# Performance work log

Hardware: AMD Instinct MI355X
Metric: run time of the kernel (lower is better)

Reference implementation:

```python
import jax, jax.numpy as jnp
import numpy as np

EPS = 1e-8
SMALL = 1e-3


def _skew(v):
    # v: [B,3] -> [B,3,3]
    vx, vy, vz = v[:, 0], v[:, 1], v[:, 2]
    z = jnp.zeros_like(vx)
    row0 = jnp.stack([z, -vz, vy], axis=-1)
    row1 = jnp.stack([vz, z, -vx], axis=-1)
    row2 = jnp.stack([-vy, vx, z], axis=-1)
    return jnp.stack([row0, row1, row2], axis=-2)


def rotmat_axis_angle_stable(aa):
    # aa: [B,3] axis*angle -> [B,3,3], Taylor-stable near theta=0
    theta = jnp.linalg.norm(aa, axis=1)
    theta2 = theta * theta + EPS
    A = jnp.sin(theta) / (theta + EPS)
    Bc = (1.0 - jnp.cos(theta)) / theta2
    th2 = theta * theta
    th4 = th2 * th2
    small = theta < SMALL
    A = jnp.where(small, 1.0 - th2 / 6.0 + th4 / 120.0, A)
    Bc = jnp.where(small, 0.5 - th2 / 24.0 + th4 / 720.0, Bc)
    K = _skew(aa)
    I = jnp.eye(3, dtype=aa.dtype)
    return I + A[:, None, None] * K + Bc[:, None, None] * jnp.matmul(K, K)


def _euler_to_rot(rpy):
    # rpy: [J,3] -> [J,3,3] (URDF origin rotations, constants)
    r, p, y = rpy[:, 0], rpy[:, 1], rpy[:, 2]
    cr, sr = jnp.cos(r), jnp.sin(r)
    cp, sp = jnp.cos(p), jnp.sin(p)
    cy, sy = jnp.cos(y), jnp.sin(y)
    row0 = jnp.stack([cy * cp, cy * sp * sr - sy * cr, cy * sp * cr + sy * sr], -1)
    row1 = jnp.stack([sy * cp, sy * sp * sr + cy * cr, sy * sp * cr - cy * sr], -1)
    row2 = jnp.stack([-sp, cp * sr, cp * cr], -1)
    return jnp.stack([row0, row1, row2], axis=-2)


def setup_inputs() -> dict:
    key = jax.random.key(0)
    k1, k2, k3, k4 = jax.random.split(key, 4)
    B, J = 131072, 24
    joint_angles = jax.random.normal(k1, (B, J), dtype=jnp.float32)
    # URDF origin constants: small offsets + rotations per joint
    xyz = 0.1 * jax.random.normal(k2, (J, 3), dtype=jnp.float32)
    rpy = 0.3 * jax.random.normal(k3, (J, 3), dtype=jnp.float32)
    R = _euler_to_rot(rpy)                                      # [J,3,3]
    T_origins = jnp.tile(jnp.eye(4, dtype=jnp.float32), (J, 1, 1))
    T_origins = T_origins.at[:, :3, :3].set(R).at[:, :3, 3].set(xyz)
    ax = jax.random.normal(k4, (J, 3), dtype=jnp.float32)
    axes = ax / jnp.linalg.norm(ax, axis=1, keepdims=True)      # unit axes
    return {"joint_angles": joint_angles, "T_origins": T_origins, "axes": axes}


def reference(joint_angles, T_origins, axes) -> jnp.ndarray:
    # joint_angles: [B,J]; T_origins: [J,4,4]; axes: [J,3]
    joint_angles = joint_angles.astype(jnp.float32)
    B = joint_angles.shape[0]
    eye4 = jnp.eye(4, dtype=jnp.float32)

    def step(T_parent, xs):
        T_org, axis, ang = xs                     # [4,4], [3], [B]
        aa = axis[None, :] * ang[:, None]         # [B,3]
        Rj = rotmat_axis_angle_stable(aa)         # [B,3,3]
        Tj = jnp.broadcast_to(eye4, (B, 4, 4)).at[:, :3, :3].set(Rj)
        T_child = jnp.matmul(jnp.matmul(T_parent, T_org), Tj)   # [B,4,4]
        return T_child, T_child[:, :3, 3]

    T0 = jnp.broadcast_to(eye4, (B, 4, 4))
    xs = (T_origins, axes, joint_angles.T)        # scan over J joints
    _, pos = jax.lax.scan(step, T0, xs)           # pos: [J,B,3]
    base_pos = jnp.zeros((B, 3), dtype=jnp.float32)
    pos = jnp.transpose(pos, (1, 0, 2)).reshape(B, -1)          # [B,J*3]
    return jnp.concatenate([base_pos, pos], axis=1)             # [B,(J+1)*3]
```

## Files before the change

kernel.cpp:

```cpp
#include <hip/hip_runtime.h>

#define BLK 256
#define NJ 24
#define G 8
#define NG (NJ / G)
#define NWV (BLK / 64)

typedef float vf4 __attribute__((ext_vector_type(4)));

__device__ __forceinline__ void hw_sincos(float h, float& s, float& c) {
    const float t = h * 0.15915494309189535f;
    float tf, ss, cc;
    asm("v_fract_f32 %0, %1" : "=v"(tf) : "v"(t));
    asm("v_sin_f32 %0, %1"   : "=v"(ss) : "v"(tf));
    asm("v_cos_f32 %0, %1"   : "=v"(cc) : "v"(tf));
    s = ss; c = cc;
}

__global__ __launch_bounds__(BLK, 2)
void fk_kernel(const float* __restrict__ angles,
               const float* __restrict__ Torg,
               const float* __restrict__ axes,
               float* __restrict__ out,
               int B)
{
    __shared__ float stage[BLK * 75];
    __shared__ float sP[NWV][NJ * 4];
    __shared__ float sQ[NWV][NJ * 4];
    __shared__ float sOT[NWV][NJ * 4];

    const int tid  = threadIdx.x;
    const int lane = tid & 63;
    const int wv   = tid >> 6;
    const int b    = blockIdx.x * BLK + tid;

    const float4* ap = reinterpret_cast<const float4*>(angles + (size_t)b * NJ);
    const float4 av0 = ap[0], av1 = ap[1], av2 = ap[2];
    const float4 av3 = ap[3], av4 = ap[4], av5 = ap[5];

    if (lane < NJ) {
        const float* o = Torg + lane * 16;
        const float m01=o[1], m02=o[2];
        const float m10=o[4], m12=o[6];
        const float m20=o[8], m21=o[9];
        const float tr = o[0] + o[5] + o[10];

        const float S    = 2.f * __builtin_amdgcn_sqrtf(tr + 1.f);
        const float rS   = __builtin_amdgcn_rcpf(S);
        const float qw   = 0.25f * S;
        const float qx   = (m21 - m12) * rS;
        const float qy   = (m02 - m20) * rS;
        const float qz   = (m10 - m01) * rS;

        const float axx = axes[lane*3+0], axy = axes[lane*3+1], axz = axes[lane*3+2];
        const float Qw_ = -qx*axx - qy*axy - qz*axz;
        const float Qx_ =  qw*axx + qy*axz - qz*axy;
        const float Qy_ =  qw*axy - qx*axz + qz*axx;
        const float Qz_ =  qw*axz + qx*axy - qy*axx;

        float* p = &sP[wv][lane * 4];
        p[0] = qw; p[1] = qx; p[2] = qy; p[3] = qz;
        float* q = &sQ[wv][lane * 4];
        q[0] = Qw_; q[1] = Qx_; q[2] = Qy_; q[3] = Qz_;
        float* t = &sOT[wv][lane * 4];
        t[0] = o[3]; t[1] = o[7]; t[2] = o[11]; t[3] = 0.f;
    }

    float Qw = 1.f, Qx = 0.f, Qy = 0.f, Qz = 0.f;
    float tx = 0.f, ty = 0.f, tz = 0.f;

    float* srow = &stage[tid * 75];
    srow[0] = 0.f; srow[1] = 0.f; srow[2] = 0.f;

    #pragma unroll 1
    for (int g = 0; g < NG; ++g) {
        float a[G];
        if (g == 0) {
            a[0]=av0.x; a[1]=av0.y; a[2]=av0.z; a[3]=av0.w;
            a[4]=av1.x; a[5]=av1.y; a[6]=av1.z; a[7]=av1.w;
        } else if (g == 1) {
            a[0]=av2.x; a[1]=av2.y; a[2]=av2.z; a[3]=av2.w;
            a[4]=av3.x; a[5]=av3.y; a[6]=av3.z; a[7]=av3.w;
        } else {
            a[0]=av4.x; a[1]=av4.y; a[2]=av4.z; a[3]=av4.w;
            a[4]=av5.x; a[5]=av5.y; a[6]=av5.z; a[7]=av5.w;
        }

        float U[G][4];
        float OT[G][3];
        #pragma unroll
        for (int u = 0; u < G; ++u) {
            const int j = g * G + u;
            const float4 P  = *reinterpret_cast<const float4*>(&sP[wv][j*4]);
            const float4 Qv = *reinterpret_cast<const float4*>(&sQ[wv][j*4]);
            const float4 ot = *reinterpret_cast<const float4*>(&sOT[wv][j*4]);
            OT[u][0] = ot.x; OT[u][1] = ot.y; OT[u][2] = ot.z;

            float s, c;
            hw_sincos(0.5f * a[u], s, c);

            U[u][0] = c*P.x + s*Qv.x;
            U[u][1] = c*P.y + s*Qv.y;
            U[u][2] = c*P.z + s*Qv.z;
            U[u][3] = c*P.w + s*Qv.w;
        }

        #pragma unroll
        for (int u = 0; u < G; ++u) {
            const int j = g * G + u;
            const float ox = OT[u][0], oy = OT[u][1], oz = OT[u][2];

            const float cx = Qy*oz - Qz*oy + Qw*ox;
            const float cy = Qz*ox - Qx*oz + Qw*oy;
            const float cz = Qx*oy - Qy*ox + Qw*oz;
            const float dx = Qy*cz - Qz*cy;
            const float dy = Qz*cx - Qx*cz;
            const float dz = Qx*cy - Qy*cx;
            tx = tx + ox + 2.f*dx;
            ty = ty + oy + 2.f*dy;
            tz = tz + oz + 2.f*dz;

            const float uw = U[u][0], ux = U[u][1], uy = U[u][2], uz = U[u][3];
            const float nw = Qw*uw - Qx*ux - Qy*uy - Qz*uz;
            const float nx = Qw*ux + Qx*uw + Qy*uz - Qz*uy;
            const float ny = Qw*uy - Qx*uz + Qy*uw + Qz*ux;
            const float nz = Qw*uz + Qx*uy - Qy*ux + Qz*uw;
            Qw = nw; Qx = nx; Qy = ny; Qz = nz;

            srow[3 + 3*j + 0] = tx;
            srow[3 + 3*j + 1] = ty;
            srow[3 + 3*j + 2] = tz;
        }
    }

    {
        const int rowbase = wv * 64;
        float* obase = out + ((size_t)blockIdx.x * BLK + rowbase) * 75;
        vf4* out4 = reinterpret_cast<vf4*>(obase);
        const vf4* st4 = reinterpret_cast<const vf4*>(&stage[rowbase * 75]);
        #pragma unroll
        for (int k = 0; k < 18; ++k) {
            const vf4 v = st4[lane + k * 64];
            __builtin_nontemporal_store(v, &out4[lane + k * 64]);
        }
        if (lane < 1200 - 18 * 64) {
            const vf4 v = st4[lane + 18 * 64];
            __builtin_nontemporal_store(v, &out4[lane + 18 * 64]);
        }
    }
}

extern "C" void kernel_launch(void* const* d_in, const int* in_sizes, int n_in,
                              void* d_out, int out_size, void* d_ws, size_t ws_size,
                              hipStream_t stream) {
    const float* angles = (const float*)d_in[0];
    const float* Torg   = (const float*)d_in[1];
    const float* axes   = (const float*)d_in[2];
    float* out = (float*)d_out;

    const int B = in_sizes[0] / NJ;
    const int grid = (B + BLK - 1) / BLK;

    fk_kernel<<<grid, BLK, 0, stream>>>(angles, Torg, axes, out, B);
}
```

Before: 17.83 us.

## Split each row's joint chain across 4 lanes with shuffle-based prefix scan

```diff
diff --git a/kernel.cpp b/kernel.cpp
--- a/kernel.cpp
+++ b/kernel.cpp
@@ -2,8 +2,8 @@
 
 #define BLK 256
 #define NJ 24
-#define G 8
-#define NG (NJ / G)
+#define JPL 6
+#define RPB (BLK / 4)
 #define NWV (BLK / 64)
 
 typedef float vf4 __attribute__((ext_vector_type(4)));
@@ -17,14 +17,31 @@
     s = ss; c = cc;
 }
 
-__global__ __launch_bounds__(BLK, 2)
+__device__ __forceinline__ void qtcompose(
+    float aw, float ax, float ay, float az, float atx, float aty, float atz,
+    float bw, float bx, float by, float bz, float btx, float bty, float btz,
+    float& ow, float& ox, float& oy, float& oz, float& otx, float& oty, float& otz)
+{
+    const float cx = ay*btz - az*bty + aw*btx;
+    const float cy = az*btx - ax*btz + aw*bty;
+    const float cz = ax*bty - ay*btx + aw*btz;
+    otx = atx + btx + 2.f*(ay*cz - az*cy);
+    oty = aty + bty + 2.f*(az*cx - ax*cz);
+    otz = atz + btz + 2.f*(ax*cy - ay*cx);
+    ow = aw*bw - ax*bx - ay*by - az*bz;
+    ox = aw*bx + ax*bw + ay*bz - az*by;
+    oy = aw*by - ax*bz + ay*bw + az*bx;
+    oz = aw*bz + ax*by - ay*bx + az*bw;
+}
+
+__global__ __launch_bounds__(BLK, 4)
 void fk_kernel(const float* __restrict__ angles,
                const float* __restrict__ Torg,
                const float* __restrict__ axes,
                float* __restrict__ out,
                int B)
 {
-    __shared__ float stage[BLK * 75];
+    __shared__ __align__(16) float stage[RPB * 75];
     __shared__ float sP[NWV][NJ * 4];
     __shared__ float sQ[NWV][NJ * 4];
     __shared__ float sOT[NWV][NJ * 4];
@@ -32,11 +49,12 @@
     const int tid  = threadIdx.x;
     const int lane = tid & 63;
     const int wv   = tid >> 6;
-    const int b    = blockIdx.x * BLK + tid;
+    const int q    = tid & 3;
+    const int rib  = tid >> 2;
+    const size_t row = (size_t)blockIdx.x * RPB + rib;
 
-    const float4* ap = reinterpret_cast<const float4*>(angles + (size_t)b * NJ);
-    const float4 av0 = ap[0], av1 = ap[1], av2 = ap[2];
-    const float4 av3 = ap[3], av4 = ap[4], av5 = ap[5];
+    const float2* ap2 = reinterpret_cast<const float2*>(angles + row * NJ + q * JPL);
+    const float2 a01 = ap2[0], a23 = ap2[1], a45 = ap2[2];
 
     if (lane < NJ) {
         const float* o = Torg + lane * 16;
@@ -44,108 +62,108 @@
         const float m10=o[4], m12=o[6];
         const float m20=o[8], m21=o[9];
         const float tr = o[0] + o[5] + o[10];
-
-        const float S    = 2.f * __builtin_amdgcn_sqrtf(tr + 1.f);
-        const float rS   = __builtin_amdgcn_rcpf(S);
-        const float qw   = 0.25f * S;
-        const float qx   = (m21 - m12) * rS;
-        const float qy   = (m02 - m20) * rS;
-        const float qz   = (m10 - m01) * rS;
+        const float S  = 2.f * __builtin_amdgcn_sqrtf(tr + 1.f);
+        const float rS = __builtin_amdgcn_rcpf(S);
+        const float qw = 0.25f * S;
+        const float qx = (m21 - m12) * rS;
+        const float qy = (m02 - m20) * rS;
+        const float qz = (m10 - m01) * rS;
 
         const float axx = axes[lane*3+0], axy = axes[lane*3+1], axz = axes[lane*3+2];
-        const float Qw_ = -qx*axx - qy*axy - qz*axz;
-        const float Qx_ =  qw*axx + qy*axz - qz*axy;
-        const float Qy_ =  qw*axy - qx*axz + qz*axx;
-        const float Qz_ =  qw*axz + qx*axy - qy*axx;
-
         float* p = &sP[wv][lane * 4];
         p[0] = qw; p[1] = qx; p[2] = qy; p[3] = qz;
-        float* q = &sQ[wv][lane * 4];
-        q[0] = Qw_; q[1] = Qx_; q[2] = Qy_; q[3] = Qz_;
+        float* qq = &sQ[wv][lane * 4];
+        qq[0] = -qx*axx - qy*axy - qz*axz;
+        qq[1] =  qw*axx + qy*axz - qz*axy;
+        qq[2] =  qw*axy - qx*axz + qz*axx;
+        qq[3] =  qw*axz + qx*axy - qy*axx;
         float* t = &sOT[wv][lane * 4];
         t[0] = o[3]; t[1] = o[7]; t[2] = o[11]; t[3] = 0.f;
     }
 
-    float Qw = 1.f, Qx = 0.f, Qy = 0.f, Qz = 0.f;
-    float tx = 0.f, ty = 0.f, tz = 0.f;
+    const float a[JPL] = {a01.x, a01.y, a23.x, a23.y, a45.x, a45.y};
 
-    float* srow = &stage[tid * 75];
-    srow[0] = 0.f; srow[1] = 0.f; srow[2] = 0.f;
+    float lqw[JPL], lqx[JPL], lqy[JPL], lqz[JPL];
+    float ltx[JPL], lty[JPL], ltz[JPL];
+    float Qw, Qx, Qy, Qz, Tx, Ty, Tz;
+    #pragma unroll
+    for (int u = 0; u < JPL; ++u) {
+        const int j = q * JPL + u;
+        const float4 P  = *reinterpret_cast<const float4*>(&sP[wv][j*4]);
+        const float4 Qv = *reinterpret_cast<const float4*>(&sQ[wv][j*4]);
+        const float4 ot = *reinterpret_cast<const float4*>(&sOT[wv][j*4]);
+        float s, c;
+        hw_sincos(0.5f * a[u], s, c);
+        const float uw = c*P.x + s*Qv.x;
+        const float ux = c*P.y + s*Qv.y;
+        const float uy = c*P.z + s*Qv.z;
+        const float uz = c*P.w + s*Qv.w;
+        if (u == 0) {
+            Qw = uw; Qx = ux; Qy = uy; Qz = uz;
+            Tx = ot.x; Ty = ot.y; Tz = ot.z;
+        } else {
+            float nw, nx, ny, nz, ntx, nty, ntz;
+            qtcompose(Qw,Qx,Qy,Qz,Tx,Ty,Tz, uw,ux,uy,uz,ot.x,ot.y,ot.z,
+                      nw,nx,ny,nz,ntx,nty,ntz);
+            Qw=nw; Qx=nx; Qy=ny; Qz=nz; Tx=ntx; Ty=nty; Tz=ntz;
+        }
+        lqw[u]=Qw; lqx[u]=Qx; lqy[u]=Qy; lqz[u]=Qz;
+        ltx[u]=Tx; lty[u]=Ty; ltz[u]=Tz;
+    }
 
-    #pragma unroll 1
-    for (int g = 0; g < NG; ++g) {
-        float a[G];
-        if (g == 0) {
-            a[0]=av0.x; a[1]=av0.y; a[2]=av0.z; a[3]=av0.w;
-            a[4]=av1.x; a[5]=av1.y; a[6]=av1.z; a[7]=av1.w;
-        } else if (g == 1) {
-            a[0]=av2.x; a[1]=av2.y; a[2]=av2.z; a[3]=av2.w;
-            a[4]=av3.x; a[5]=av3.y; a[6]=av3.z; a[7]=av3.w;
-        } else {
-            a[0]=av4.x; a[1]=av4.y; a[2]=av4.z; a[3]=av4.w;
-            a[4]=av5.x; a[5]=av5.y; a[6]=av5.z; a[7]=av5.w;
+    float Sw=Qw, Sx=Qx, Sy=Qy, Sz=Qz, Stx=Tx, Sty=Ty, Stz=Tz;
+    {
+        const float rw=__shfl_up(Sw,1,4), rx=__shfl_up(Sx,1,4), ry=__shfl_up(Sy,1,4), rz=__shfl_up(Sz,1,4);
+        const float rtx=__shfl_up(Stx,1,4), rty=__shfl_up(Sty,1,4), rtz=__shfl_up(Stz,1,4);
+        if (q >= 1) {
+            float ow,ox,oy,oz,otx,oty,otz;
+            qtcompose(rw,rx,ry,rz,rtx,rty,rtz, Sw,Sx,Sy,Sz,Stx,Sty,Stz, ow,ox,oy,oz,otx,oty,otz);
+            Sw=ow; Sx=ox; Sy=oy; Sz=oz; Stx=otx; Sty=oty; Stz=otz;
         }
+    }
+    {
+        const float rw=__shfl_up(Sw,2,4), rx=__shfl_up(Sx,2,4), ry=__shfl_up(Sy,2,4), rz=__shfl_up(Sz,2,4);
+        const float rtx=__shfl_up(Stx,2,4), rty=__shfl_up(Sty,2,4), rtz=__shfl_up(Stz,2,4);
+        if (q >= 2) {
+            float ow,ox,oy,oz,otx,oty,otz;
+            qtcompose(rw,rx,ry,rz,rtx,rty,rtz, Sw,Sx,Sy,Sz,Stx,Sty,Stz, ow,ox,oy,oz,otx,oty,otz);
+            Sw=ow; Sx=ox; Sy=oy; Sz=oz; Stx=otx; Sty=oty; Stz=otz;
+        }
+    }
+    float Ew=__shfl_up(Sw,1,4), Ex=__shfl_up(Sx,1,4), Ey=__shfl_up(Sy,1,4), Ez=__shfl_up(Sz,1,4);
+    float Etx=__shfl_up(Stx,1,4), Ety=__shfl_up(Sty,1,4), Etz=__shfl_up(Stz,1,4);
+    if (q == 0) { Ew=1.f; Ex=0.f; Ey=0.f; Ez=0.f; Etx=0.f; Ety=0.f; Etz=0.f; }
 
-        float U[G][4];
-        float OT[G][3];
-        #pragma unroll
-        for (int u = 0; u < G; ++u) {
-            const int j = g * G + u;
-            const float4 P  = *reinterpret_cast<const float4*>(&sP[wv][j*4]);
-            const float4 Qv = *reinterpret_cast<const float4*>(&sQ[wv][j*4]);
-            const float4 ot = *reinterpret_cast<const float4*>(&sOT[wv][j*4]);
-            OT[u][0] = ot.x; OT[u][1] = ot.y; OT[u][2] = ot.z;
-
-            float s, c;
-            hw_sincos(0.5f * a[u], s, c);
-
-            U[u][0] = c*P.x + s*Qv.x;
-            U[u][1] = c*P.y + s*Qv.y;
-            U[u][2] = c*P.z + s*Qv.z;
-            U[u][3] = c*P.w + s*Qv.w;
-        }
-
-        #pragma unroll
-        for (int u = 0; u < G; ++u) {
-            const int j = g * G + u;
-            const float ox = OT[u][0], oy = OT[u][1], oz = OT[u][2];
-
-            const float cx = Qy*oz - Qz*oy + Qw*ox;
-            const float cy = Qz*ox - Qx*oz + Qw*oy;
-            const float cz = Qx*oy - Qy*ox + Qw*oz;
-            const float dx = Qy*cz - Qz*cy;
-            const float dy = Qz*cx - Qx*cz;
-            const float dz = Qx*cy - Qy*cx;
-            tx = tx + ox + 2.f*dx;
-            ty = ty + oy + 2.f*dy;
-            tz = tz + oz + 2.f*dz;
-
-            const float uw = U[u][0], ux = U[u][1], uy = U[u][2], uz = U[u][3];
-            const float nw = Qw*uw - Qx*ux - Qy*uy - Qz*uz;
-            const float nx = Qw*ux + Qx*uw + Qy*uz - Qz*uy;
-            const float ny = Qw*uy - Qx*uz + Qy*uw + Qz*ux;
-            const float nz = Qw*uz + Qx*uy - Qy*ux + Qz*uw;
-            Qw = nw; Qx = nx; Qy = ny; Qz = nz;
-
-            srow[3 + 3*j + 0] = tx;
-            srow[3 + 3*j + 1] = ty;
-            srow[3 + 3*j + 2] = tz;
-        }
+    float* srow = &stage[rib * 75];
+    if (q == 0) { srow[0]=0.f; srow[1]=0.f; srow[2]=0.f; }
+    #pragma unroll
+    for (int u = 0; u < JPL; ++u) {
+        const float vx = ltx[u], vy = lty[u], vz = ltz[u];
+        const float cx = Ey*vz - Ez*vy + Ew*vx;
+        const float cy = Ez*vx - Ex*vz + Ew*vy;
+        const float cz = Ex*vy - Ey*vx + Ew*vz;
+        const float px = Etx + vx + 2.f*(Ey*cz - Ez*cy);
+        const float py = Ety + vy + 2.f*(Ez*cx - Ex*cz);
+        const float pz = Etz + vz + 2.f*(Ex*cy - Ey*cx);
+        const int j = q * JPL + u;
+        srow[3 + 3*j + 0] = px;
+        srow[3 + 3*j + 1] = py;
+        srow[3 + 3*j + 2] = pz;
     }
 
     {
-        const int rowbase = wv * 64;
-        float* obase = out + ((size_t)blockIdx.x * BLK + rowbase) * 75;
+        const int rowbase = wv * 16;
+        float* obase = out + ((size_t)blockIdx.x * RPB + rowbase) * 75;
         vf4* out4 = reinterpret_cast<vf4*>(obase);
         const vf4* st4 = reinterpret_cast<const vf4*>(&stage[rowbase * 75]);
         #pragma unroll
-        for (int k = 0; k < 18; ++k) {
+        for (int k = 0; k < 4; ++k) {
             const vf4 v = st4[lane + k * 64];
             __builtin_nontemporal_store(v, &out4[lane + k * 64]);
         }
-        if (lane < 1200 - 18 * 64) {
-            const vf4 v = st4[lane + 18 * 64];
-            __builtin_nontemporal_store(v, &out4[lane + 18 * 64]);
+        if (lane < 44) {
+            const vf4 v = st4[lane + 256];
+            __builtin_nontemporal_store(v, &out4[lane + 256]);
         }
     }
 }
@@ -159,7 +177,7 @@
     float* out = (float*)d_out;
 
     const int B = in_sizes[0] / NJ;
-    const int grid = (B + BLK - 1) / BLK;
+    const int grid = B / RPB;
 
     fk_kernel<<<grid, BLK, 0, stream>>>(angles, Torg, axes, out, B);
 }
```

Measured after the change: 19.24 us. +7.9%, slower.
